# Kernel tuning notes

Hardware: AMD Instinct MI355X
Metric: run time of the kernel (lower is better)

The kernel has to match this reference:

```python
import jax, jax.numpy as jnp
import numpy as np

B, L, HID = 8, 1025, 1024
H, KV, DH = 16, 4, 64
EPS = 1e-6
ROPE_BASE = 10000.0


def _rms_norm(x, w):
    var = jnp.mean(jnp.square(x), axis=-1, keepdims=True)
    return x * jax.lax.rsqrt(var + EPS) * w


def _rotate_half(x):
    x1, x2 = jnp.split(x, 2, axis=-1)
    return jnp.concatenate([-x2, x1], axis=-1)


def _rope_cache(seq_len, dim):
    inv_freq = 1.0 / (ROPE_BASE ** (jnp.arange(0, dim, 2, dtype=jnp.float32) / dim))
    pos = jnp.arange(seq_len, dtype=jnp.float32)
    freqs = pos[:, None] * inv_freq[None, :]            # [L_img, dim/2]
    emb = jnp.concatenate([freqs, freqs], axis=-1)       # [L_img, dim]
    return jnp.cos(emb), jnp.sin(emb)


def setup_inputs() -> dict:
    key = jax.random.key(0)
    ks = jax.random.split(key, 5)
    s_in = 1.0
    s_q = float(np.sqrt(2.0 / (HID + H * DH)))
    s_kv = float(np.sqrt(2.0 / (HID + KV * DH)))
    s_o = float(np.sqrt(2.0 / (H * DH + HID)) / np.sqrt(2.0))
    return {
        "inputs": jax.random.normal(ks[0], (B, L, HID), jnp.float32) * s_in,
        "Wq": jax.random.normal(ks[1], (H * DH, HID), jnp.float32) * s_q,
        "Wk": jax.random.normal(ks[2], (KV * DH, HID), jnp.float32) * s_kv,
        "Wv": jax.random.normal(ks[3], (KV * DH, HID), jnp.float32) * s_kv,
        "Wo": jax.random.normal(ks[4], (HID, H * DH), jnp.float32) * s_o,
        "q_norm_w": jnp.ones((DH,), jnp.float32),
        "k_norm_w": jnp.ones((DH,), jnp.float32),
    }


def reference(inputs, Wq, Wk, Wv, Wo, q_norm_w, k_norm_w):
    b, l, _ = inputs.shape
    # projections (torch Linear: x @ W.T), reshape to heads, QK RMSNorm
    q = (inputs @ Wq.T).reshape(b, l, H, DH)
    k = (inputs @ Wk.T).reshape(b, l, KV, DH)
    v = (inputs @ Wv.T).reshape(b, l, KV, DH)
    q = _rms_norm(q, q_norm_w).transpose(0, 2, 1, 3)    # [B,H,L,DH]
    k = _rms_norm(k, k_norm_w).transpose(0, 2, 1, 3)    # [B,KV,L,DH]
    v = v.transpose(0, 2, 1, 3)                          # [B,KV,L,DH]

    # RoPE only on image tokens (skip first action token)
    l_img = l - 1
    cos, sin = _rope_cache(l_img, DH)                    # [L_img, DH]
    cos = cos[None, None].astype(q.dtype)
    sin = sin[None, None].astype(q.dtype)
    q_img = q[:, :, 1:]
    k_img = k[:, :, 1:]
    q = jnp.concatenate([q[:, :, :1], q_img * cos + _rotate_half(q_img) * sin], axis=2)
    k = jnp.concatenate([k[:, :, :1], k_img * cos + _rotate_half(k_img) * sin], axis=2)

    # GQA: repeat kv heads
    rep = H // KV
    k = jnp.repeat(k, rep, axis=1)                       # [B,H,L,DH]
    v = jnp.repeat(v, rep, axis=1)

    # manual attention: NOTE no 1/sqrt(DH) scaling (faithful to source)
    scores = jnp.einsum("bhqd,bhkd->bhqk", q, k)
    attn = jax.nn.softmax(scores.astype(jnp.float32), axis=-1).astype(q.dtype)
    out = jnp.einsum("bhqk,bhkd->bhqd", attn, v)         # [B,H,L,DH]
    out = out.transpose(0, 2, 1, 3).reshape(b, l, H * DH)
    return out @ Wo.T
```

## Files before the change

kernel.cpp:

```cpp
#include <hip/hip_runtime.h>
#include <hip/hip_bf16.h>

using bf16 = __hip_bfloat16;
typedef __bf16 bf16x8 __attribute__((ext_vector_type(8)));
typedef float f32x4 __attribute__((ext_vector_type(4)));
typedef short short8 __attribute__((ext_vector_type(8)));
typedef unsigned short ushort4v __attribute__((ext_vector_type(4)));

#define MFMA16(a, b, c) __builtin_amdgcn_mfma_f32_16x16x32_bf16((a), (b), (c), 0, 0, 0)

constexpr int B_ = 8, L_ = 1025, H_ = 16, KV_ = 4;
constexpr int LKP_ = 1088;
constexpr int M_ = B_ * L_;

template <int NWG>
__device__ __forceinline__ int xcd_swz(int orig) {
  constexpr int q = NWG >> 3, r = NWG & 7;
  const int x = orig & 7, idx = orig >> 3;
  return (x < r ? x * (q + 1) : r * (q + 1) + (x - r) * q) + idx;
}

__global__ __launch_bounds__(64) void detect_dtype(const unsigned short* qw_raw,
                                                   int* flag) {
  if (threadIdx.x == 0) flag[0] = (qw_raw[0] == 0x3F80) ? 0 : 1;
}

__global__ __launch_bounds__(256) void zero_pads(bf16* Kb, bf16* VT) {
  const int idx = blockIdx.x * 256 + threadIdx.x;
  const bf16 z = __float2bfloat16(0.f);
  {
    const int g = idx / 4032, rem = idx % 4032;
    const int r = rem >> 6, d = rem & 63;
    Kb[((size_t)g * LKP_ + 1025 + r) * 64 + d] = z;
  }
  {
    const int row = idx / 63, c = idx % 63;
    VT[(size_t)row * LKP_ + 1025 + c] = z;
  }
}

template <int EPI, int NT, int NWG>
__global__ __launch_bounds__(512) void gemm_bt(
    const void* __restrict__ Xv, const void* __restrict__ W0v,
    const void* __restrict__ W1v, const void* __restrict__ W2v,
    void* __restrict__ O0, bf16* __restrict__ O1, bf16* __restrict__ O2,
    const void* __restrict__ qwv, const void* __restrict__ kwv,
    const int* __restrict__ flag) {
  const int f32in = *flag;
  const int wg = xcd_swz<NWG>(blockIdx.x);
  const int m0 = (wg / NT) * 128;
  const int n0 = (wg % NT) * 128;

  const void* Wv;
  int nw0;
  if constexpr (EPI == 0) {
    Wv = W0v; nw0 = n0;
  } else {
    if (n0 < 1024)      { Wv = W0v; nw0 = n0; }
    else if (n0 < 1280) { Wv = W1v; nw0 = n0 - 1024; }
    else                { Wv = W2v; nw0 = n0 - 1280; }
  }

  const bool af32 = (EPI == 1) && (f32in != 0);
  const bool bf32 = (f32in != 0);

  __shared__ bf16 As[2][128 * 32];
  __shared__ bf16 Bs[2][128 * 32];

  const int tid = threadIdx.x;
  const int lane = tid & 63, wid = tid >> 6;
  const int wr = wid >> 1, wc = wid & 1;
  const int lo = lane & 15, g = lane >> 4;

  const f32x4 zero4 = {0.f, 0.f, 0.f, 0.f};
  f32x4 acc[2][4];
#pragma unroll
  for (int i = 0; i < 2; ++i)
#pragma unroll
    for (int j = 0; j < 4; ++j) acc[i][j] = zero4;

  const int rr = tid >> 2, cb = tid & 3;
  const int wofs = rr * 32 + ((cb ^ ((rr >> 1) & 3)) * 8);
  int xr = m0 + rr; if (xr > M_ - 1) xr = M_ - 1;
  const char* xp = (const char*)Xv + ((size_t)xr * 1024 + cb * 8) * (af32 ? 4 : 2);
  const char* wp = (const char*)Wv + ((size_t)(nw0 + rr) * 1024 + cb * 8) * (bf32 ? 4 : 2);
  const int xstep = af32 ? 128 : 64;
  const int wstep = bf32 ? 128 : 64;

  f32x4 ra0, ra1, rb0, rb1;
  auto loadA = [&] {
    ra0 = *(const f32x4*)xp;
    if (af32) ra1 = *(const f32x4*)(xp + 16);
    xp += xstep;
  };
  auto loadB = [&] {
    rb0 = *(const f32x4*)wp;
    if (bf32) rb1 = *(const f32x4*)(wp + 16);
    wp += wstep;
  };
  auto packA = [&]() -> short8 {
    if (af32) {
      short8 o;
#pragma unroll
      for (int j = 0; j < 4; ++j) {
        o[j]     = __builtin_bit_cast(short, __float2bfloat16(ra0[j]));
        o[j + 4] = __builtin_bit_cast(short, __float2bfloat16(ra1[j]));
      }
      return o;
    }
    return __builtin_bit_cast(short8, ra0);
  };
  auto packB = [&]() -> short8 {
    if (bf32) {
      short8 o;
#pragma unroll
      for (int j = 0; j < 4; ++j) {
        o[j]     = __builtin_bit_cast(short, __float2bfloat16(rb0[j]));
        o[j + 4] = __builtin_bit_cast(short, __float2bfloat16(rb1[j]));
      }
      return o;
    }
    return __builtin_bit_cast(short8, rb0);
  };

  loadA(); loadB();

  const int swl = (g ^ ((lo >> 1) & 3)) * 8;

  for (int kt = 0; kt < 32; ++kt) {
    const int cur = kt & 1;
    __syncthreads();
    *reinterpret_cast<short8*>(&As[cur][wofs]) = packA();
    *reinterpret_cast<short8*>(&Bs[cur][wofs]) = packB();
    __syncthreads();

    if (kt < 31) {
      loadA(); loadB();
    }

    bf16x8 a[2], bb[4];
#pragma unroll
    for (int i = 0; i < 2; ++i)
      a[i] = *reinterpret_cast<const bf16x8*>(&As[cur][(wr * 32 + i * 16 + lo) * 32 + swl]);
#pragma unroll
    for (int j = 0; j < 4; ++j)
      bb[j] = *reinterpret_cast<const bf16x8*>(&Bs[cur][(wc * 64 + j * 16 + lo) * 32 + swl]);
#pragma unroll
    for (int i = 0; i < 2; ++i)
#pragma unroll
      for (int j = 0; j < 4; ++j)
        acc[i][j] = MFMA16(a[i], bb[j], acc[i][j]);
  }

  const bool qkreg = (EPI == 1) && (n0 < 1280);
  float wv[4];
  float invf0 = 0.f, invf1 = 0.f;
  if (qkreg) {
    const void* w = (n0 < 1024) ? qwv : kwv;
#pragma unroll
    for (int j = 0; j < 4; ++j) {
      float wf = f32in ? ((const float*)w)[j * 16 + lo]
                       : __bfloat162float(((const bf16*)w)[j * 16 + lo]);
      wv[j] = __bfloat162float(__float2bfloat16(wf));
    }
    constexpr float c = -0.41524101186092029f;
    invf0 = exp2f((float)lo * c);
    invf1 = invf0 * exp2f(16.f * c);
  }

#pragma unroll
  for (int i = 0; i < 2; ++i) {
#pragma unroll
    for (int ii = 0; ii < 4; ++ii) {
      const int m = m0 + wr * 32 + i * 16 + g * 4 + ii;
      if (m >= M_) continue;
      const int b = m / L_;
      const int l = m % L_;
      float fv[4];
#pragma unroll
      for (int j = 0; j < 4; ++j) fv[j] = acc[i][j][ii];

      if (qkreg) {
#pragma unroll
        for (int j = 0; j < 4; ++j)
          fv[j] = __bfloat162float(__float2bfloat16(fv[j]));
        float ss = fv[0] * fv[0] + fv[1] * fv[1] + fv[2] * fv[2] + fv[3] * fv[3];
        ss += __shfl_xor(ss, 1);
        ss += __shfl_xor(ss, 2);
        ss += __shfl_xor(ss, 4);
        ss += __shfl_xor(ss, 8);
        const float r = rsqrtf(ss * (1.f / 64.f) + 1e-6f);
#pragma unroll
        for (int j = 0; j < 4; ++j) fv[j] *= r * wv[j];
        if (l > 0) {
          const float pos = (float)(l - 1);
          float sn0, cs0, sn1, cs1;
          __sincosf(pos * invf0, &sn0, &cs0);
          __sincosf(pos * invf1, &sn1, &cs1);
          const float a0 = fv[0], a2 = fv[2];
          fv[0] = a0 * cs0 - a2 * sn0;
          fv[2] = a2 * cs0 + a0 * sn0;
          const float a1 = fv[1], a3 = fv[3];
          fv[1] = a1 * cs1 - a3 * sn1;
          fv[3] = a3 * cs1 + a1 * sn1;
        }
      }

#pragma unroll
      for (int j = 0; j < 4; ++j) {
        const int n = n0 + wc * 64 + j * 16 + lo;
        const float f = fv[j];
        if constexpr (EPI == 0) {
          if (f32in) ((float*)O0)[(size_t)m * 1024 + n] = f;
          else       ((bf16*)O0)[(size_t)m * 1024 + n] = __float2bfloat16(f);
        } else {
          const bf16 v = __float2bfloat16(f);
          if (n < 1024) {
            ((bf16*)O0)[((size_t)(b * H_ + (n >> 6)) * L_ + l) * 64 + (n & 63)] = v;
          } else if (n < 1280) {
            const int c2 = n - 1024;
            O1[((size_t)(b * KV_ + (c2 >> 6)) * LKP_ + l) * 64 + (c2 & 63)] = v;
          } else {
            const int c2 = n - 1280;
            O2[((size_t)(b * KV_ + (c2 >> 6)) * 64 + (c2 & 63)) * LKP_ + l] = v;
          }
        }
      }
    }
  }
}

__global__ __launch_bounds__(512) void attn(
    const bf16* __restrict__ Q, const bf16* __restrict__ Kt,
    const bf16* __restrict__ VT, bf16* __restrict__ AO) {
  const int tid = threadIdx.x, lane = tid & 63, w = tid >> 6;
  const int lo = lane & 15, g = lane >> 4;
  const int qt = blockIdx.x, h = blockIdx.y, b = blockIdx.z;
  const int kv = h >> 2;

  __shared__ unsigned short Ks[64 * 64];
  __shared__ unsigned short Vs[64 * 64];
  __shared__ unsigned short Ps[8 * 16 * 64];

  const bf16* qbase = Q + (size_t)(b * H_ + h) * L_ * 64;
  int qrow = qt * 128 + w * 16 + lo;
  if (qrow > L_ - 1) qrow = L_ - 1;
  const bf16x8 qf0 = *reinterpret_cast<const bf16x8*>(qbase + (size_t)qrow * 64 + g * 8);
  const bf16x8 qf1 = *reinterpret_cast<const bf16x8*>(qbase + (size_t)qrow * 64 + 32 + g * 8);

  const f32x4 zero4 = {0.f, 0.f, 0.f, 0.f};
  f32x4 o[4];
  float mi = -3e38f, li = 0.f;
#pragma unroll
  for (int i = 0; i < 4; ++i) o[i] = zero4;

  const int sr = tid >> 3;
  const int scol = (tid & 7) * 8;
  const int swcol = ((tid & 7) ^ (sr & 7)) * 8;
  const bf16* kptr = Kt + ((size_t)(b * KV_ + kv) * LKP_ + sr) * 64 + scol;
  const bf16* vptr = VT + ((size_t)(b * KV_ + kv) * 64 + sr) * LKP_ + scol;

  const int sw0 = (g ^ (lo & 7)) * 8;
  const int sw1 = ((4 | g) ^ (lo & 7)) * 8;

  short8 ka = *reinterpret_cast<const short8*>(kptr);
  short8 va = *reinterpret_cast<const short8*>(vptr);

  for (int kt = 0; kt < 17; ++kt) {
    __syncthreads();
    *reinterpret_cast<short8*>(&Ks[sr * 64 + swcol]) = ka;
    *reinterpret_cast<short8*>(&Vs[sr * 64 + swcol]) = va;
    __syncthreads();

    if (kt < 16) {
      kptr += 64 * 64;
      vptr += 64;
      ka = *reinterpret_cast<const short8*>(kptr);
      va = *reinterpret_cast<const short8*>(vptr);
    }

    f32x4 s[4];
    __builtin_amdgcn_s_setprio(1);
#pragma unroll
    for (int kb = 0; kb < 4; ++kb) {
      f32x4 t = zero4;
      const bf16x8 ka0 = *reinterpret_cast<const bf16x8*>(&Ks[(kb * 16 + lo) * 64 + sw0]);
      const bf16x8 ka1 = *reinterpret_cast<const bf16x8*>(&Ks[(kb * 16 + lo) * 64 + sw1]);
      t = MFMA16(ka0, qf0, t);
      t = MFMA16(ka1, qf1, t);
      s[kb] = t;
    }
    __builtin_amdgcn_s_setprio(0);
    if (kt == 16) {
#pragma unroll
      for (int kb = 0; kb < 4; ++kb)
#pragma unroll
        for (int i = 0; i < 4; ++i)
          if (kt * 64 + kb * 16 + g * 4 + i >= L_) s[kb][i] = -1e30f;
    }

    float t0 = fmaxf(fmaxf(s[0][0], s[0][1]), fmaxf(s[0][2], s[0][3]));
    float t1 = fmaxf(fmaxf(s[1][0], s[1][1]), fmaxf(s[1][2], s[1][3]));
    float t2 = fmaxf(fmaxf(s[2][0], s[2][1]), fmaxf(s[2][2], s[2][3]));
    float t3 = fmaxf(fmaxf(s[3][0], s[3][1]), fmaxf(s[3][2], s[3][3]));
    float tm = fmaxf(fmaxf(t0, t1), fmaxf(t2, t3));
    tm = fmaxf(tm, __shfl_xor(tm, 16));
    tm = fmaxf(tm, __shfl_xor(tm, 32));
    if (!__all(tm <= mi)) {
      const float mn = fmaxf(mi, tm);
      const float sc = __expf(mi - mn);
      mi = mn;
      li *= sc;
#pragma unroll
      for (int db = 0; db < 4; ++db)
#pragma unroll
        for (int i = 0; i < 4; ++i) o[db][i] *= sc;
    }
#pragma unroll
    for (int kb = 0; kb < 4; ++kb)
#pragma unroll
      for (int i = 0; i < 4; ++i) s[kb][i] = __expf(s[kb][i] - mi);
    float p0 = (s[0][0] + s[0][1]) + (s[0][2] + s[0][3]);
    float p1 = (s[1][0] + s[1][1]) + (s[1][2] + s[1][3]);
    float p2 = (s[2][0] + s[2][1]) + (s[2][2] + s[2][3]);
    float p3 = (s[3][0] + s[3][1]) + (s[3][2] + s[3][3]);
    float ps = (p0 + p1) + (p2 + p3);
    ps += __shfl_xor(ps, 16);
    ps += __shfl_xor(ps, 32);
    li += ps;

#pragma unroll
    for (int kb = 0; kb < 4; ++kb) {
      ushort4v pk;
#pragma unroll
      for (int i = 0; i < 4; ++i)
        pk[i] = __builtin_bit_cast(unsigned short, __float2bfloat16(s[kb][i]));
      const int pblk = (2 * kb + (g >> 1)) ^ (lo & 7);
      *reinterpret_cast<ushort4v*>(&Ps[w * 1024 + lo * 64 + pblk * 8 + (g & 1) * 4]) = pk;
    }

    const bf16x8 pb0 = *reinterpret_cast<const bf16x8*>(&Ps[w * 1024 + lo * 64 + sw0]);
    const bf16x8 pb1 = *reinterpret_cast<const bf16x8*>(&Ps[w * 1024 + lo * 64 + sw1]);
    __builtin_amdgcn_s_setprio(1);
#pragma unroll
    for (int db = 0; db < 4; ++db) {
      const bf16x8 va0 = *reinterpret_cast<const bf16x8*>(&Vs[(db * 16 + lo) * 64 + sw0]);
      const bf16x8 va1 = *reinterpret_cast<const bf16x8*>(&Vs[(db * 16 + lo) * 64 + sw1]);
      o[db] = MFMA16(va0, pb0, o[db]);
      o[db] = MFMA16(va1, pb1, o[db]);
    }
    __builtin_amdgcn_s_setprio(0);
  }

  const int qr = qt * 128 + w * 16 + lo;
  if (qr < L_) {
    const float inv = 1.f / li;
    unsigned* base = (unsigned*)(AO + ((size_t)b * L_ + qr) * 1024 + h * 64);
#pragma unroll
    for (int db = 0; db < 4; ++db) {
#pragma unroll
      for (int i2 = 0; i2 < 4; i2 += 2) {
        const unsigned u0 = __builtin_bit_cast(unsigned short,
                                __float2bfloat16(o[db][i2] * inv));
        const unsigned u1 = __builtin_bit_cast(unsigned short,
                                __float2bfloat16(o[db][i2 + 1] * inv));
        base[(db * 16 + 4 * g + i2) >> 1] = u0 | (u1 << 16);
      }
    }
  }
}

extern "C" void kernel_launch(void* const* d_in, const int* in_sizes, int n_in,
                              void* d_out, int out_size, void* d_ws, size_t ws_size,
                              hipStream_t stream) {
  (void)in_sizes; (void)n_in; (void)out_size; (void)ws_size;

  char* wsb = (char*)d_ws;
  int* flagp = (int*)wsb;
  bf16* Qb  = (bf16*)(wsb + 16);
  bf16* Kb  = Qb  + (size_t)B_ * H_ * L_ * 64;
  bf16* VTb = Kb  + (size_t)B_ * KV_ * LKP_ * 64;
  bf16* AOb = VTb + (size_t)B_ * KV_ * 64 * LKP_;

  detect_dtype<<<1, 64, 0, stream>>>((const unsigned short*)d_in[5], flagp);
  zero_pads<<<504, 256, 0, stream>>>(Kb, VTb);

  gemm_bt<1, 12, 780><<<780, 512, 0, stream>>>(
      d_in[0], d_in[1], d_in[2], d_in[3], Qb, Kb, VTb, d_in[5], d_in[6], flagp);
  attn<<<dim3(9, 16, 8), 512, 0, stream>>>(Qb, Kb, VTb, AOb);
  gemm_bt<0, 8, 520><<<520, 512, 0, stream>>>(
      AOb, d_in[4], nullptr, nullptr, d_out, nullptr, nullptr, nullptr, nullptr,
      flagp);
}
```

Measured before the change: 217.7 us.

## Enlarge GEMM tiles to 256-row blocks and add direct global-to-LDS loads

```diff
diff --git a/kernel.cpp b/kernel.cpp
--- a/kernel.cpp
+++ b/kernel.cpp
@@ -12,6 +12,12 @@
 constexpr int B_ = 8, L_ = 1025, H_ = 16, KV_ = 4;
 constexpr int LKP_ = 1088;
 constexpr int M_ = B_ * L_;
+
+__device__ __forceinline__ void gl_lds16(const bf16* g, bf16* l) {
+  __builtin_amdgcn_global_load_lds(
+      (const __attribute__((address_space(1))) void*)g,
+      (__attribute__((address_space(3))) void*)l, 16, 0, 0);
+}
 
 template <int NWG>
 __device__ __forceinline__ int xcd_swz(int orig) {
@@ -39,17 +45,19 @@
   }
 }
 
-template <int EPI, int NT, int NWG>
+template <int EPI, int BN, int NT, int NWG>
 __global__ __launch_bounds__(512) void gemm_bt(
     const void* __restrict__ Xv, const void* __restrict__ W0v,
     const void* __restrict__ W1v, const void* __restrict__ W2v,
     void* __restrict__ O0, bf16* __restrict__ O1, bf16* __restrict__ O2,
     const void* __restrict__ qwv, const void* __restrict__ kwv,
     const int* __restrict__ flag) {
+  constexpr int NJ = BN / 64;
+  constexpr int NBCH = BN / 64;
   const int f32in = *flag;
   const int wg = xcd_swz<NWG>(blockIdx.x);
-  const int m0 = (wg / NT) * 128;
-  const int n0 = (wg % NT) * 128;
+  const int m0 = (wg / NT) * 256;
+  const int n0 = (wg % NT) * BN;
 
   const void* Wv;
   int nw0;
@@ -61,95 +69,125 @@
     else                { Wv = W2v; nw0 = n0 - 1280; }
   }
 
-  const bool af32 = (EPI == 1) && (f32in != 0);
-  const bool bf32 = (f32in != 0);
-
-  __shared__ bf16 As[2][128 * 32];
-  __shared__ bf16 Bs[2][128 * 32];
+  __shared__ bf16 As[2][256 * 64];
+  __shared__ bf16 Bs[2][BN * 64];
 
   const int tid = threadIdx.x;
   const int lane = tid & 63, wid = tid >> 6;
-  const int wr = wid >> 1, wc = wid & 1;
+  const int wr = wid >> 2, wc = wid & 3;
   const int lo = lane & 15, g = lane >> 4;
 
   const f32x4 zero4 = {0.f, 0.f, 0.f, 0.f};
-  f32x4 acc[2][4];
-#pragma unroll
-  for (int i = 0; i < 2; ++i)
-#pragma unroll
-    for (int j = 0; j < 4; ++j) acc[i][j] = zero4;
-
-  const int rr = tid >> 2, cb = tid & 3;
-  const int wofs = rr * 32 + ((cb ^ ((rr >> 1) & 3)) * 8);
-  int xr = m0 + rr; if (xr > M_ - 1) xr = M_ - 1;
-  const char* xp = (const char*)Xv + ((size_t)xr * 1024 + cb * 8) * (af32 ? 4 : 2);
-  const char* wp = (const char*)Wv + ((size_t)(nw0 + rr) * 1024 + cb * 8) * (bf32 ? 4 : 2);
-  const int xstep = af32 ? 128 : 64;
-  const int wstep = bf32 ? 128 : 64;
-
-  f32x4 ra0, ra1, rb0, rb1;
-  auto loadA = [&] {
-    ra0 = *(const f32x4*)xp;
-    if (af32) ra1 = *(const f32x4*)(xp + 16);
-    xp += xstep;
+  f32x4 acc[8][NJ];
+#pragma unroll
+  for (int i = 0; i < 8; ++i)
+#pragma unroll
+    for (int j = 0; j < NJ; ++j) acc[i][j] = zero4;
+
+  const int trow = tid >> 3;
+  const int scol8 = (((tid & 7) ^ (trow & 7)) * 8);
+  const int dofs = trow * 64 + (tid & 7) * 8;
+
+  const bf16* ap[4];
+  const bf16* bp[NBCH];
+  if (!f32in || EPI == 0) {
+#pragma unroll
+    for (int c = 0; c < 4; ++c) {
+      int xr = m0 + trow + c * 64; if (xr > M_ - 1) xr = M_ - 1;
+      ap[c] = (const bf16*)Xv + (size_t)xr * 1024 + scol8;
+    }
+  }
+  if (!f32in) {
+#pragma unroll
+    for (int c = 0; c < NBCH; ++c)
+      bp[c] = (const bf16*)Wv + (size_t)(nw0 + trow + c * 64) * 1024 + scol8;
+  }
+
+  auto stageG = [&](int buf) {
+#pragma unroll
+    for (int c = 0; c < 4; ++c) {
+      gl_lds16(ap[c], &As[buf][c * 4096 + dofs]);
+      ap[c] += 64;
+    }
+#pragma unroll
+    for (int c = 0; c < NBCH; ++c) {
+      gl_lds16(bp[c], &Bs[buf][c * 4096 + dofs]);
+      bp[c] += 64;
+    }
   };
-  auto loadB = [&] {
-    rb0 = *(const f32x4*)wp;
-    if (bf32) rb1 = *(const f32x4*)(wp + 16);
-    wp += wstep;
+
+  auto compute = [&](int buf) {
+#pragma unroll
+    for (int kk = 0; kk < 2; ++kk) {
+      const int swz = (((kk << 2) | g) ^ (lo & 7)) * 8;
+      bf16x8 bb[NJ];
+#pragma unroll
+      for (int j = 0; j < NJ; ++j)
+        bb[j] = *reinterpret_cast<const bf16x8*>(
+            &Bs[buf][(wc * (BN / 4) + j * 16 + lo) * 64 + swz]);
+#pragma unroll
+      for (int i = 0; i < 8; ++i) {
+        const bf16x8 a = *reinterpret_cast<const bf16x8*>(
+            &As[buf][(wr * 128 + i * 16 + lo) * 64 + swz]);
+#pragma unroll
+        for (int j = 0; j < NJ; ++j)
+          acc[i][j] = MFMA16(a, bb[j], acc[i][j]);
+      }
+    }
   };
-  auto packA = [&]() -> short8 {
-    if (af32) {
-      short8 o;
-#pragma unroll
-      for (int j = 0; j < 4; ++j) {
-        o[j]     = __builtin_bit_cast(short, __float2bfloat16(ra0[j]));
-        o[j + 4] = __builtin_bit_cast(short, __float2bfloat16(ra1[j]));
-      }
-      return o;
-    }
-    return __builtin_bit_cast(short8, ra0);
-  };
-  auto packB = [&]() -> short8 {
-    if (bf32) {
-      short8 o;
-#pragma unroll
-      for (int j = 0; j < 4; ++j) {
-        o[j]     = __builtin_bit_cast(short, __float2bfloat16(rb0[j]));
-        o[j + 4] = __builtin_bit_cast(short, __float2bfloat16(rb1[j]));
-      }
-      return o;
-    }
-    return __builtin_bit_cast(short8, rb0);
-  };
-
-  loadA(); loadB();
-
-  const int swl = (g ^ ((lo >> 1) & 3)) * 8;
-
-  for (int kt = 0; kt < 32; ++kt) {
-    const int cur = kt & 1;
-    __syncthreads();
-    *reinterpret_cast<short8*>(&As[cur][wofs]) = packA();
-    *reinterpret_cast<short8*>(&Bs[cur][wofs]) = packB();
-    __syncthreads();
-
-    if (kt < 31) {
-      loadA(); loadB();
-    }
-
-    bf16x8 a[2], bb[4];
-#pragma unroll
-    for (int i = 0; i < 2; ++i)
-      a[i] = *reinterpret_cast<const bf16x8*>(&As[cur][(wr * 32 + i * 16 + lo) * 32 + swl]);
-#pragma unroll
-    for (int j = 0; j < 4; ++j)
-      bb[j] = *reinterpret_cast<const bf16x8*>(&Bs[cur][(wc * 64 + j * 16 + lo) * 32 + swl]);
-#pragma unroll
-    for (int i = 0; i < 2; ++i)
-#pragma unroll
-      for (int j = 0; j < 4; ++j)
-        acc[i][j] = MFMA16(a[i], bb[j], acc[i][j]);
+
+  if (!f32in) {
+    stageG(0);
+    asm volatile("s_waitcnt vmcnt(0)" ::: "memory");
+    __builtin_amdgcn_s_barrier();
+    for (int kt = 0; kt < 16; ++kt) {
+      const int cur = kt & 1;
+      if (kt < 15) stageG(cur ^ 1);
+      compute(cur);
+      asm volatile("s_waitcnt vmcnt(0)" ::: "memory");
+      __builtin_amdgcn_s_barrier();
+    }
+  } else {
+    const bool af32 = (EPI == 1);
+    for (int kt = 0; kt < 16; ++kt) {
+      short8 ra[4], rb[NBCH];
+#pragma unroll
+      for (int c = 0; c < 4; ++c) {
+        int xr = m0 + trow + c * 64; if (xr > M_ - 1) xr = M_ - 1;
+        const size_t off = (size_t)xr * 1024 + scol8 + kt * 64;
+        if (af32) {
+          const f32x4 v0 = *((const f32x4*)Xv + off / 4);
+          const f32x4 v1 = *((const f32x4*)Xv + off / 4 + 1);
+#pragma unroll
+          for (int j = 0; j < 4; ++j) {
+            ra[c][j]     = __builtin_bit_cast(short, __float2bfloat16(v0[j]));
+            ra[c][j + 4] = __builtin_bit_cast(short, __float2bfloat16(v1[j]));
+          }
+        } else {
+          ra[c] = *reinterpret_cast<const short8*>((const bf16*)Xv + off);
+        }
+      }
+#pragma unroll
+      for (int c = 0; c < NBCH; ++c) {
+        const size_t off = (size_t)(nw0 + trow + c * 64) * 1024 + scol8 + kt * 64;
+        const f32x4 v0 = *((const f32x4*)Wv + off / 4);
+        const f32x4 v1 = *((const f32x4*)Wv + off / 4 + 1);
+#pragma unroll
+        for (int j = 0; j < 4; ++j) {
+          rb[c][j]     = __builtin_bit_cast(short, __float2bfloat16(v0[j]));
+          rb[c][j + 4] = __builtin_bit_cast(short, __float2bfloat16(v1[j]));
+        }
+      }
+      __syncthreads();
+#pragma unroll
+      for (int c = 0; c < 4; ++c)
+        *reinterpret_cast<short8*>(&As[0][c * 4096 + dofs]) = ra[c];
+#pragma unroll
+      for (int c = 0; c < NBCH; ++c)
+        *reinterpret_cast<short8*>(&Bs[0][c * 4096 + dofs]) = rb[c];
+      __syncthreads();
+      compute(0);
+    }
   }
 
   const bool qkreg = (EPI == 1) && (n0 < 1280);
@@ -169,46 +207,50 @@
   }
 
 #pragma unroll
-  for (int i = 0; i < 2; ++i) {
+  for (int i = 0; i < 8; ++i) {
 #pragma unroll
     for (int ii = 0; ii < 4; ++ii) {
-      const int m = m0 + wr * 32 + i * 16 + g * 4 + ii;
+      const int m = m0 + wr * 128 + i * 16 + g * 4 + ii;
       if (m >= M_) continue;
       const int b = m / L_;
       const int l = m % L_;
-      float fv[4];
-#pragma unroll
-      for (int j = 0; j < 4; ++j) fv[j] = acc[i][j][ii];
-
-      if (qkreg) {
-#pragma unroll
-        for (int j = 0; j < 4; ++j)
-          fv[j] = __bfloat162float(__float2bfloat16(fv[j]));
-        float ss = fv[0] * fv[0] + fv[1] * fv[1] + fv[2] * fv[2] + fv[3] * fv[3];
-        ss += __shfl_xor(ss, 1);
-        ss += __shfl_xor(ss, 2);
-        ss += __shfl_xor(ss, 4);
-        ss += __shfl_xor(ss, 8);
-        const float r = rsqrtf(ss * (1.f / 64.f) + 1e-6f);
-#pragma unroll
-        for (int j = 0; j < 4; ++j) fv[j] *= r * wv[j];
-        if (l > 0) {
-          const float pos = (float)(l - 1);
-          float sn0, cs0, sn1, cs1;
-          __sincosf(pos * invf0, &sn0, &cs0);
-          __sincosf(pos * invf1, &sn1, &cs1);
-          const float a0 = fv[0], a2 = fv[2];
-          fv[0] = a0 * cs0 - a2 * sn0;
-          fv[2] = a2 * cs0 + a0 * sn0;
-          const float a1 = fv[1], a3 = fv[3];
-          fv[1] = a1 * cs1 - a3 * sn1;
-          fv[3] = a3 * cs1 + a1 * sn1;
+      float fv[NJ];
+#pragma unroll
+      for (int j = 0; j < NJ; ++j) fv[j] = acc[i][j][ii];
+
+      if constexpr (EPI == 1) {
+        if (qkreg) {
+#pragma unroll
+          for (int j = 0; j < NJ; ++j)
+            fv[j] = __bfloat162float(__float2bfloat16(fv[j]));
+          float ss = 0.f;
+#pragma unroll
+          for (int j = 0; j < NJ; ++j) ss += fv[j] * fv[j];
+          ss += __shfl_xor(ss, 1);
+          ss += __shfl_xor(ss, 2);
+          ss += __shfl_xor(ss, 4);
+          ss += __shfl_xor(ss, 8);
+          const float r = rsqrtf(ss * (1.f / 64.f) + 1e-6f);
+#pragma unroll
+          for (int j = 0; j < NJ; ++j) fv[j] *= r * wv[j];
+          if (l > 0) {
+            const float pos = (float)(l - 1);
+            float sn0, cs0, sn1, cs1;
+            __sincosf(pos * invf0, &sn0, &cs0);
+            __sincosf(pos * invf1, &sn1, &cs1);
+            const float a0 = fv[0], a2 = fv[2];
+            fv[0] = a0 * cs0 - a2 * sn0;
+            fv[2] = a2 * cs0 + a0 * sn0;
+            const float a1 = fv[1], a3 = fv[3];
+            fv[1] = a1 * cs1 - a3 * sn1;
+            fv[3] = a3 * cs1 + a1 * sn1;
+          }
         }
       }
 
 #pragma unroll
-      for (int j = 0; j < 4; ++j) {
-        const int n = n0 + wc * 64 + j * 16 + lo;
+      for (int j = 0; j < NJ; ++j) {
+        const int n = n0 + wc * (BN / 4) + j * 16 + lo;
         const float f = fv[j];
         if constexpr (EPI == 0) {
           if (f32in) ((float*)O0)[(size_t)m * 1024 + n] = f;
@@ -385,10 +427,10 @@
   detect_dtype<<<1, 64, 0, stream>>>((const unsigned short*)d_in[5], flagp);
   zero_pads<<<504, 256, 0, stream>>>(Kb, VTb);
 
-  gemm_bt<1, 12, 780><<<780, 512, 0, stream>>>(
+  gemm_bt<1, 256, 6, 198><<<198, 512, 0, stream>>>(
       d_in[0], d_in[1], d_in[2], d_in[3], Qb, Kb, VTb, d_in[5], d_in[6], flagp);
   attn<<<dim3(9, 16, 8), 512, 0, stream>>>(Qb, Kb, VTb, AOb);
-  gemm_bt<0, 8, 520><<<520, 512, 0, stream>>>(
+  gemm_bt<0, 128, 8, 264><<<264, 512, 0, stream>>>(
       AOb, d_in[4], nullptr, nullptr, d_out, nullptr, nullptr, nullptr, nullptr,
       flagp);
 }
```

Result: slower. 225.3 us (+3.5%).

## Pre-pack weights into MFMA fragment layout and stage full A panel in LDS

Applied to the files above, without the earlier changes.

```diff
diff --git a/kernel.cpp b/kernel.cpp
--- a/kernel.cpp
+++ b/kernel.cpp
@@ -12,6 +12,12 @@
 constexpr int B_ = 8, L_ = 1025, H_ = 16, KV_ = 4;
 constexpr int LKP_ = 1088;
 constexpr int M_ = B_ * L_;
+
+__device__ __forceinline__ void gl_lds16(const bf16* g, bf16* l) {
+  __builtin_amdgcn_global_load_lds(
+      (const __attribute__((address_space(1))) void*)g,
+      (__attribute__((address_space(3))) void*)l, 16, 0, 0);
+}
 
 template <int NWG>
 __device__ __forceinline__ int xcd_swz(int orig) {
@@ -39,133 +45,153 @@
   }
 }
 
-template <int EPI, int NT, int NWG>
-__global__ __launch_bounds__(512) void gemm_bt(
-    const void* __restrict__ Xv, const void* __restrict__ W0v,
-    const void* __restrict__ W1v, const void* __restrict__ W2v,
+__global__ __launch_bounds__(256) void pack_w(
+    const void* __restrict__ Wq, const void* __restrict__ Wk,
+    const void* __restrict__ Wv, const void* __restrict__ Wo,
+    bf16* __restrict__ Wf3, bf16* __restrict__ WfO,
+    const int* __restrict__ flag) {
+  const int f = *flag;
+  const int t = blockIdx.x * 256 + threadIdx.x;
+  int j, kk, lane, rowbase;
+  const void* src;
+  bf16* dst;
+  if (t < 196608) {
+    j = t >> 11; kk = (t >> 6) & 31; lane = t & 63;
+    dst = Wf3 + (size_t)t * 8;
+    if (j < 64)      { src = Wq; rowbase = j * 16; }
+    else if (j < 80) { src = Wk; rowbase = (j - 64) * 16; }
+    else             { src = Wv; rowbase = (j - 80) * 16; }
+  } else {
+    const int t2 = t - 196608;
+    j = t2 >> 11; kk = (t2 >> 6) & 31; lane = t2 & 63;
+    dst = WfO + (size_t)t2 * 8;
+    src = Wo; rowbase = j * 16;
+  }
+  const int row = rowbase + (lane & 15);
+  const int k0 = kk * 32 + (lane >> 4) * 8;
+  const size_t off = (size_t)row * 1024 + k0;
+  short8 o;
+  if (f) {
+    const f32x4 v0 = *reinterpret_cast<const f32x4*>((const float*)src + off);
+    const f32x4 v1 = *reinterpret_cast<const f32x4*>((const float*)src + off + 4);
+#pragma unroll
+    for (int e = 0; e < 4; ++e) {
+      o[e]     = __builtin_bit_cast(short, __float2bfloat16(v0[e]));
+      o[e + 4] = __builtin_bit_cast(short, __float2bfloat16(v1[e]));
+    }
+  } else {
+    o = *reinterpret_cast<const short8*>((const bf16*)src + off);
+  }
+  *reinterpret_cast<short8*>(dst) = o;
+}
+
+template <int EPI, int NJ, int NWG>
+__global__ __launch_bounds__(512) void gemm_sb(
+    const void* __restrict__ Xv, const bf16* __restrict__ Wf,
     void* __restrict__ O0, bf16* __restrict__ O1, bf16* __restrict__ O2,
     const void* __restrict__ qwv, const void* __restrict__ kwv,
     const int* __restrict__ flag) {
   const int f32in = *flag;
   const int wg = xcd_swz<NWG>(blockIdx.x);
-  const int m0 = (wg / NT) * 128;
-  const int n0 = (wg % NT) * 128;
-
-  const void* Wv;
-  int nw0;
-  if constexpr (EPI == 0) {
-    Wv = W0v; nw0 = n0;
+  const int m0 = (wg % 129) * 64;
+  const int n0 = (wg / 129) * (NJ * 64);
+
+  __shared__ bf16 As[64 * 1024];
+
+  const int tid = threadIdx.x, lane = tid & 63, wid = tid >> 6;
+  const int wr = wid >> 2, wc = wid & 3;
+  const int lo = lane & 15, g = lane >> 4;
+
+  if ((EPI == 0) || !f32in) {
+    const bf16* Xb = (const bf16*)Xv;
+#pragma unroll
+    for (int s = 0; s < 16; ++s) {
+      const int q = tid + s * 512;
+      const int r = q >> 7, c = q & 127;
+      int xr = m0 + r; if (xr > M_ - 1) xr = M_ - 1;
+      gl_lds16(Xb + (size_t)xr * 1024 + ((c ^ (r & 7)) * 8),
+               &As[r * 1024 + c * 8]);
+    }
   } else {
-    if (n0 < 1024)      { Wv = W0v; nw0 = n0; }
-    else if (n0 < 1280) { Wv = W1v; nw0 = n0 - 1024; }
-    else                { Wv = W2v; nw0 = n0 - 1280; }
-  }
-
-  const bool af32 = (EPI == 1) && (f32in != 0);
-  const bool bf32 = (f32in != 0);
-
-  __shared__ bf16 As[2][128 * 32];
-  __shared__ bf16 Bs[2][128 * 32];
-
-  const int tid = threadIdx.x;
-  const int lane = tid & 63, wid = tid >> 6;
-  const int wr = wid >> 1, wc = wid & 1;
-  const int lo = lane & 15, g = lane >> 4;
+    const float* Xf = (const float*)Xv;
+#pragma unroll
+    for (int s = 0; s < 16; ++s) {
+      const int q = tid + s * 512;
+      const int r = q >> 7, c = q & 127;
+      int xr = m0 + r; if (xr > M_ - 1) xr = M_ - 1;
+      const float* sp = Xf + (size_t)xr * 1024 + ((c ^ (r & 7)) * 8);
+      const f32x4 v0 = *(const f32x4*)sp;
+      const f32x4 v1 = *(const f32x4*)(sp + 4);
+      short8 o;
+#pragma unroll
+      for (int e = 0; e < 4; ++e) {
+        o[e]     = __builtin_bit_cast(short, __float2bfloat16(v0[e]));
+        o[e + 4] = __builtin_bit_cast(short, __float2bfloat16(v1[e]));
+      }
+      *reinterpret_cast<short8*>(&As[r * 1024 + c * 8]) = o;
+    }
+  }
+  __syncthreads();
 
   const f32x4 zero4 = {0.f, 0.f, 0.f, 0.f};
-  f32x4 acc[2][4];
+  f32x4 acc[2][NJ];
 #pragma unroll
   for (int i = 0; i < 2; ++i)
 #pragma unroll
-    for (int j = 0; j < 4; ++j) acc[i][j] = zero4;
-
-  const int rr = tid >> 2, cb = tid & 3;
-  const int wofs = rr * 32 + ((cb ^ ((rr >> 1) & 3)) * 8);
-  int xr = m0 + rr; if (xr > M_ - 1) xr = M_ - 1;
-  const char* xp = (const char*)Xv + ((size_t)xr * 1024 + cb * 8) * (af32 ? 4 : 2);
-  const char* wp = (const char*)Wv + ((size_t)(nw0 + rr) * 1024 + cb * 8) * (bf32 ? 4 : 2);
-  const int xstep = af32 ? 128 : 64;
-  const int wstep = bf32 ? 128 : 64;
-
-  f32x4 ra0, ra1, rb0, rb1;
-  auto loadA = [&] {
-    ra0 = *(const f32x4*)xp;
-    if (af32) ra1 = *(const f32x4*)(xp + 16);
-    xp += xstep;
+    for (int j2 = 0; j2 < NJ; ++j2) acc[i][j2] = zero4;
+
+  const bf16* wfp = Wf + ((size_t)((n0 >> 4) + wc * NJ)) * 16384;
+
+  auto loadB = [&](bf16x8* dst, int ks) {
+#pragma unroll
+    for (int j2 = 0; j2 < NJ; ++j2)
+      dst[j2] = *reinterpret_cast<const bf16x8*>(
+          wfp + (size_t)j2 * 16384 + ks * 512 + lane * 8);
   };
-  auto loadB = [&] {
-    rb0 = *(const f32x4*)wp;
-    if (bf32) rb1 = *(const f32x4*)(wp + 16);
-    wp += wstep;
+  const int ar0 = (wr * 32 + lo) * 1024;
+  const int ar1 = (wr * 32 + 16 + lo) * 1024;
+  const int lx = lo & 7;
+  auto comp = [&](const bf16x8* bf, int ks) {
+    const int cb = ((ks * 4 + g) ^ lx) * 8;
+    const bf16x8 a0 = *reinterpret_cast<const bf16x8*>(&As[ar0 + cb]);
+    const bf16x8 a1 = *reinterpret_cast<const bf16x8*>(&As[ar1 + cb]);
+#pragma unroll
+    for (int j2 = 0; j2 < NJ; ++j2) acc[0][j2] = MFMA16(a0, bf[j2], acc[0][j2]);
+#pragma unroll
+    for (int j2 = 0; j2 < NJ; ++j2) acc[1][j2] = MFMA16(a1, bf[j2], acc[1][j2]);
   };
-  auto packA = [&]() -> short8 {
-    if (af32) {
-      short8 o;
-#pragma unroll
-      for (int j = 0; j < 4; ++j) {
-        o[j]     = __builtin_bit_cast(short, __float2bfloat16(ra0[j]));
-        o[j + 4] = __builtin_bit_cast(short, __float2bfloat16(ra1[j]));
+
+  bf16x8 bA[NJ], bB[NJ];
+  loadB(bA, 0);
+  for (int ks = 0; ks < 32; ks += 2) {
+    loadB(bB, ks + 1);
+    comp(bA, ks);
+    if (ks + 2 < 32) loadB(bA, ks + 2);
+    comp(bB, ks + 1);
+  }
+
+  constexpr int NQ = NJ / 4;
+  float invf0 = 0.f, invf1 = 0.f;
+  float wvh[NQ][4];
+  bool qk[NQ];
+  if constexpr (EPI == 1) {
+    constexpr float cc = -0.41524101186092029f;
+    invf0 = exp2f((float)lo * cc);
+    invf1 = invf0 * exp2f(16.f * cc);
+#pragma unroll
+    for (int jq = 0; jq < NQ; ++jq) {
+      const int nh = n0 + wc * (NJ * 16) + jq * 64;
+      qk[jq] = (nh < 1280);
+      if (qk[jq]) {
+        const void* w = (nh < 1024) ? qwv : kwv;
+#pragma unroll
+        for (int jj = 0; jj < 4; ++jj) {
+          float wf = f32in ? ((const float*)w)[jj * 16 + lo]
+                           : __bfloat162float(((const bf16*)w)[jj * 16 + lo]);
+          wvh[jq][jj] = __bfloat162float(__float2bfloat16(wf));
+        }
       }
-      return o;
-    }
-    return __builtin_bit_cast(short8, ra0);
-  };
-  auto packB = [&]() -> short8 {
-    if (bf32) {
-      short8 o;
-#pragma unroll
-      for (int j = 0; j < 4; ++j) {
-        o[j]     = __builtin_bit_cast(short, __float2bfloat16(rb0[j]));
-        o[j + 4] = __builtin_bit_cast(short, __float2bfloat16(rb1[j]));
-      }
-      return o;
-    }
-    return __builtin_bit_cast(short8, rb0);
-  };
-
-  loadA(); loadB();
-
-  const int swl = (g ^ ((lo >> 1) & 3)) * 8;
-
-  for (int kt = 0; kt < 32; ++kt) {
-    const int cur = kt & 1;
-    __syncthreads();
-    *reinterpret_cast<short8*>(&As[cur][wofs]) = packA();
-    *reinterpret_cast<short8*>(&Bs[cur][wofs]) = packB();
-    __syncthreads();
-
-    if (kt < 31) {
-      loadA(); loadB();
-    }
-
-    bf16x8 a[2], bb[4];
-#pragma unroll
-    for (int i = 0; i < 2; ++i)
-      a[i] = *reinterpret_cast<const bf16x8*>(&As[cur][(wr * 32 + i * 16 + lo) * 32 + swl]);
-#pragma unroll
-    for (int j = 0; j < 4; ++j)
-      bb[j] = *reinterpret_cast<const bf16x8*>(&Bs[cur][(wc * 64 + j * 16 + lo) * 32 + swl]);
-#pragma unroll
-    for (int i = 0; i < 2; ++i)
-#pragma unroll
-      for (int j = 0; j < 4; ++j)
-        acc[i][j] = MFMA16(a[i], bb[j], acc[i][j]);
-  }
-
-  const bool qkreg = (EPI == 1) && (n0 < 1280);
-  float wv[4];
-  float invf0 = 0.f, invf1 = 0.f;
-  if (qkreg) {
-    const void* w = (n0 < 1024) ? qwv : kwv;
-#pragma unroll
-    for (int j = 0; j < 4; ++j) {
-      float wf = f32in ? ((const float*)w)[j * 16 + lo]
-                       : __bfloat162float(((const bf16*)w)[j * 16 + lo]);
-      wv[j] = __bfloat162float(__float2bfloat16(wf));
-    }
-    constexpr float c = -0.41524101186092029f;
-    invf0 = exp2f((float)lo * c);
-    invf1 = invf0 * exp2f(16.f * c);
+    }
   }
 
 #pragma unroll
@@ -174,55 +200,61 @@
     for (int ii = 0; ii < 4; ++ii) {
       const int m = m0 + wr * 32 + i * 16 + g * 4 + ii;
       if (m >= M_) continue;
-      const int b = m / L_;
-      const int l = m % L_;
-      float fv[4];
-#pragma unroll
-      for (int j = 0; j < 4; ++j) fv[j] = acc[i][j][ii];
-
-      if (qkreg) {
-#pragma unroll
-        for (int j = 0; j < 4; ++j)
-          fv[j] = __bfloat162float(__float2bfloat16(fv[j]));
-        float ss = fv[0] * fv[0] + fv[1] * fv[1] + fv[2] * fv[2] + fv[3] * fv[3];
-        ss += __shfl_xor(ss, 1);
-        ss += __shfl_xor(ss, 2);
-        ss += __shfl_xor(ss, 4);
-        ss += __shfl_xor(ss, 8);
-        const float r = rsqrtf(ss * (1.f / 64.f) + 1e-6f);
-#pragma unroll
-        for (int j = 0; j < 4; ++j) fv[j] *= r * wv[j];
-        if (l > 0) {
-          const float pos = (float)(l - 1);
-          float sn0, cs0, sn1, cs1;
-          __sincosf(pos * invf0, &sn0, &cs0);
-          __sincosf(pos * invf1, &sn1, &cs1);
-          const float a0 = fv[0], a2 = fv[2];
-          fv[0] = a0 * cs0 - a2 * sn0;
-          fv[2] = a2 * cs0 + a0 * sn0;
-          const float a1 = fv[1], a3 = fv[3];
-          fv[1] = a1 * cs1 - a3 * sn1;
-          fv[3] = a3 * cs1 + a1 * sn1;
-        }
-      }
-
-#pragma unroll
-      for (int j = 0; j < 4; ++j) {
-        const int n = n0 + wc * 64 + j * 16 + lo;
-        const float f = fv[j];
-        if constexpr (EPI == 0) {
+      if constexpr (EPI == 0) {
+#pragma unroll
+        for (int j2 = 0; j2 < NJ; ++j2) {
+          const int n = n0 + wc * (NJ * 16) + j2 * 16 + lo;
+          const float f = acc[i][j2][ii];
           if (f32in) ((float*)O0)[(size_t)m * 1024 + n] = f;
           else       ((bf16*)O0)[(size_t)m * 1024 + n] = __float2bfloat16(f);
-        } else {
-          const bf16 v = __float2bfloat16(f);
-          if (n < 1024) {
-            ((bf16*)O0)[((size_t)(b * H_ + (n >> 6)) * L_ + l) * 64 + (n & 63)] = v;
-          } else if (n < 1280) {
-            const int c2 = n - 1024;
-            O1[((size_t)(b * KV_ + (c2 >> 6)) * LKP_ + l) * 64 + (c2 & 63)] = v;
-          } else {
-            const int c2 = n - 1280;
-            O2[((size_t)(b * KV_ + (c2 >> 6)) * 64 + (c2 & 63)) * LKP_ + l] = v;
+        }
+      } else {
+        const int b = m / L_;
+        const int l = m % L_;
+#pragma unroll
+        for (int jq = 0; jq < NQ; ++jq) {
+          float fv[4];
+#pragma unroll
+          for (int jj = 0; jj < 4; ++jj) fv[jj] = acc[i][jq * 4 + jj][ii];
+          const int nh = n0 + wc * (NJ * 16) + jq * 64;
+          if (qk[jq]) {
+#pragma unroll
+            for (int jj = 0; jj < 4; ++jj)
+              fv[jj] = __bfloat162float(__float2bfloat16(fv[jj]));
+            float ss = fv[0] * fv[0] + fv[1] * fv[1] + fv[2] * fv[2] + fv[3] * fv[3];
+            ss += __shfl_xor(ss, 1);
+            ss += __shfl_xor(ss, 2);
+            ss += __shfl_xor(ss, 4);
+            ss += __shfl_xor(ss, 8);
+            const float r = rsqrtf(ss * (1.f / 64.f) + 1e-6f);
+#pragma unroll
+            for (int jj = 0; jj < 4; ++jj) fv[jj] *= r * wvh[jq][jj];
+            if (l > 0) {
+              const float pos = (float)(l - 1);
+              float sn0, cs0, sn1, cs1;
+              __sincosf(pos * invf0, &sn0, &cs0);
+              __sincosf(pos * invf1, &sn1, &cs1);
+              const float a0 = fv[0], a2 = fv[2];
+              fv[0] = a0 * cs0 - a2 * sn0;
+              fv[2] = a2 * cs0 + a0 * sn0;
+              const float a1 = fv[1], a3 = fv[3];
+              fv[1] = a1 * cs1 - a3 * sn1;
+              fv[3] = a3 * cs1 + a1 * sn1;
+            }
+          }
+#pragma unroll
+          for (int jj = 0; jj < 4; ++jj) {
+            const int n = nh + jj * 16 + lo;
+            const bf16 v = __float2bfloat16(fv[jj]);
+            if (n < 1024) {
+              ((bf16*)O0)[((size_t)(b * H_ + (n >> 6)) * L_ + l) * 64 + (n & 63)] = v;
+            } else if (n < 1280) {
+              const int c2 = n - 1024;
+              O1[((size_t)(b * KV_ + (c2 >> 6)) * LKP_ + l) * 64 + (c2 & 63)] = v;
+            } else {
+              const int c2 = n - 1280;
+              O2[((size_t)(b * KV_ + (c2 >> 6)) * 64 + (c2 & 63)) * LKP_ + l] = v;
+            }
           }
         }
       }
@@ -377,18 +409,21 @@
 
   char* wsb = (char*)d_ws;
   int* flagp = (int*)wsb;
-  bf16* Qb  = (bf16*)(wsb + 16);
+  bf16* Wf3 = (bf16*)(wsb + 16);
+  bf16* WfO = Wf3 + (size_t)1536 * 1024;
+  bf16* Qb  = WfO + (size_t)1024 * 1024;
   bf16* Kb  = Qb  + (size_t)B_ * H_ * L_ * 64;
   bf16* VTb = Kb  + (size_t)B_ * KV_ * LKP_ * 64;
   bf16* AOb = VTb + (size_t)B_ * KV_ * 64 * LKP_;
 
   detect_dtype<<<1, 64, 0, stream>>>((const unsigned short*)d_in[5], flagp);
+  pack_w<<<1280, 256, 0, stream>>>(d_in[1], d_in[2], d_in[3], d_in[4],
+                                   Wf3, WfO, flagp);
   zero_pads<<<504, 256, 0, stream>>>(Kb, VTb);
 
-  gemm_bt<1, 12, 780><<<780, 512, 0, stream>>>(
-      d_in[0], d_in[1], d_in[2], d_in[3], Qb, Kb, VTb, d_in[5], d_in[6], flagp);
+  gemm_sb<1, 12, 258><<<258, 512, 0, stream>>>(
+      d_in[0], Wf3, Qb, Kb, VTb, d_in[5], d_in[6], flagp);
   attn<<<dim3(9, 16, 8), 512, 0, stream>>>(Qb, Kb, VTb, AOb);
-  gemm_bt<0, 8, 520><<<520, 512, 0, stream>>>(
-      AOb, d_in[4], nullptr, nullptr, d_out, nullptr, nullptr, nullptr, nullptr,
-      flagp);
-}
+  gemm_sb<0, 8, 258><<<258, 512, 0, stream>>>(
+      AOb, WfO, d_out, nullptr, nullptr, nullptr, nullptr, flagp);
+}
```

After: 243.8 us. 12.0% more time.
